# Performance work log

Hardware: AMD Instinct MI355X
Metric: run time of the kernel (lower is better)

The kernel has to match this reference:

```python
import jax, jax.numpy as jnp
import numpy as np

TOP_K = 2


def setup_inputs() -> dict:
    key = jax.random.key(0)
    ks = jax.random.split(key, 6)
    B, S, D, H, E = 2, 2048, 1024, 4096, 8
    s_in = 1.0 / np.sqrt(D)
    s_hid = 1.0 / np.sqrt(H)
    return {
        "x": jax.random.normal(ks[0], (B, S, D), jnp.float32),
        "Wg": jax.random.normal(ks[1], (E, D), jnp.float32) * s_in,
        "W1": jax.random.normal(ks[2], (E, D, H), jnp.float32) * s_in,
        "b1": jax.random.normal(ks[3], (E, H), jnp.float32) * 0.01,
        "W2": jax.random.normal(ks[4], (E, H, D), jnp.float32) * s_hid,
        "b2": jax.random.normal(ks[5], (E, D), jnp.float32) * 0.01,
    }


def reference(x, Wg, W1, b1, W2, b2):
    B, S, D = x.shape
    E = Wg.shape[0]
    T = B * S
    xf = x.reshape(T, D)

    # ---- router ----
    logits = xf @ Wg.T                              # (T, E)
    probs = jax.nn.softmax(logits, axis=-1)
    top_v, top_i = jax.lax.top_k(probs, TOP_K)      # (T, k)
    top_v = top_v / top_v.sum(axis=-1, keepdims=True)

    # aux load-balancing loss
    expert_mask = jax.nn.one_hot(top_i, E, dtype=probs.dtype).sum(axis=1)  # (T, E)
    f = expert_mask.mean(axis=0)
    p = probs.mean(axis=0)
    aux_loss = E * (f * p).sum()

    # ---- combine weights: scatter normalized top-k probs into (T, E) ----
    w = jnp.zeros((T, E), probs.dtype).at[jnp.arange(T)[:, None], top_i].add(top_v)

    # ---- all-expert FFN (grouped GEMM form), weighted combine ----
    h = jax.nn.silu(jnp.einsum('td,edh->teh', xf, W1) + b1[None])   # (T, E, H)
    y = jnp.einsum('teh,ehd->ted', h, W2) + b2[None]                # (T, E, D)
    out = jnp.einsum('ted,te->td', y, w)                            # (T, D)
    return out.reshape(B, S, D), aux_loss
```

## Files before the change

### kernel.cpp

```cpp
#include <hip/hip_runtime.h>
#include <cstdint>
#include <cstddef>

#define T_TOK 4096
#define DIM   1024
#define HID   4096
#define NE    8
#define PAD   128
#define PADMAX 9216

typedef _Float16 half_t;
typedef __attribute__((ext_vector_type(8))) _Float16 half8;
typedef __attribute__((ext_vector_type(4))) float floatx4;

__device__ __forceinline__ float silu_f(float v) {
  return v / (1.0f + expf(-v));
}

__device__ __forceinline__ half8 cvt44(float4 a, float4 b) {
  half8 o;
  o[0] = (half_t)a.x; o[1] = (half_t)a.y; o[2] = (half_t)a.z; o[3] = (half_t)a.w;
  o[4] = (half_t)b.x; o[5] = (half_t)b.y; o[6] = (half_t)b.z; o[7] = (half_t)b.w;
  return o;
}

__device__ __forceinline__ void gload16(const void* g, void* l) {
  __builtin_amdgcn_global_load_lds(
      (const __attribute__((address_space(1))) unsigned int*)g,
      (__attribute__((address_space(3))) unsigned int*)l, 16, 0, 0);
}

__global__ void k_reset(float* prob_sum, unsigned* cnt, unsigned* cursor,
                        int* pair_tok, float* pair_wt) {
  int i = blockIdx.x * 256 + threadIdx.x;
  if (i < PADMAX) { pair_tok[i] = 0; pair_wt[i] = 0.0f; }
  if (i < NE) { prob_sum[i] = 0.0f; cnt[i] = 0u; cursor[i] = 0u; }
}

__global__ __launch_bounds__(256) void k_cvt_x(const float* __restrict__ x,
                                               half_t* __restrict__ xh) {
  size_t i = (size_t)blockIdx.x * 256 + threadIdx.x;
  const float4* s = (const float4*)(x + i * 8);
  float4 a = s[0], b = s[1];
  *(half8*)(xh + i * 8) = cvt44(a, b);
}

__global__ __launch_bounds__(256) void k_tr_w1(const float* __restrict__ W1,
                                               half_t* __restrict__ W1t,
                                               int j0, int Hc) {
  __shared__ half_t T[64][72];
  int e = blockIdx.z, h0 = blockIdx.x * 64, d0 = blockIdx.y * 64;
  int tid = threadIdx.x;
  {
    int r = tid >> 2, c16 = (tid & 3) * 16;
    const float* s = W1 + ((size_t)e * DIM + d0 + r) * HID + j0 + h0 + c16;
    float4 a = ((const float4*)s)[0], b = ((const float4*)s)[1];
    float4 c = ((const float4*)s)[2], d = ((const float4*)s)[3];
    *(half8*)&T[r][c16] = cvt44(a, b);
    *(half8*)&T[r][c16 + 8] = cvt44(c, d);
  }
  __syncthreads();
  {
    int n = tid >> 2, d16 = (tid & 3) * 16;
    half8 u, v;
#pragma unroll
    for (int j = 0; j < 8; ++j) { u[j] = T[d16 + j][n]; v[j] = T[d16 + 8 + j][n]; }
    half_t* dst = W1t + ((size_t)e * Hc + h0 + n) * DIM + d0 + d16;
    *(half8*)dst = u;
    *(half8*)(dst + 8) = v;
  }
}

__global__ __launch_bounds__(256) void k_tr_w2(const float* __restrict__ W2,
                                               half_t* __restrict__ W2t,
                                               int j0, int Hc) {
  __shared__ half_t T[64][72];
  int e = blockIdx.z, d0 = blockIdx.x * 64, h0 = blockIdx.y * 64;
  int tid = threadIdx.x;
  {
    int r = tid >> 2, c16 = (tid & 3) * 16;
    const float* s = W2 + ((size_t)e * HID + j0 + h0 + r) * DIM + d0 + c16;
    float4 a = ((const float4*)s)[0], b = ((const float4*)s)[1];
    float4 c = ((const float4*)s)[2], d = ((const float4*)s)[3];
    *(half8*)&T[r][c16] = cvt44(a, b);
    *(half8*)&T[r][c16 + 8] = cvt44(c, d);
  }
  __syncthreads();
  {
    int n = tid >> 2, h16 = (tid & 3) * 16;
    half8 u, v;
#pragma unroll
    for (int j = 0; j < 8; ++j) { u[j] = T[h16 + j][n]; v[j] = T[h16 + 8 + j][n]; }
    half_t* dst = W2t + ((size_t)e * DIM + d0 + n) * Hc + h0 + h16;
    *(half8*)dst = u;
    *(half8*)(dst + 8) = v;
  }
}

__global__ __launch_bounds__(256) void k_router(
    const float* __restrict__ x, const float* __restrict__ Wg,
    int* __restrict__ top_i, float* __restrict__ top_w,
    float* __restrict__ prob_sum, unsigned* __restrict__ cnt) {
  __shared__ float sWg[NE * DIM];
  __shared__ float sProb[NE];
  __shared__ unsigned sCnt[NE];
  int tid = threadIdx.x;
  if (tid < NE) { sProb[tid] = 0.0f; sCnt[tid] = 0u; }
  for (int i = tid; i < NE * DIM; i += 256) sWg[i] = Wg[i];
  __syncthreads();

  int wave = tid >> 6, lane = tid & 63;
  for (int it = 0; it < 4; ++it) {
    int t = blockIdx.x * 16 + wave * 4 + it;
    const float* xp = x + (size_t)t * DIM;
    float acc[NE];
#pragma unroll
    for (int e = 0; e < NE; ++e) acc[e] = 0.0f;
    for (int i = 0; i < DIM / 64; ++i) {
      int d = i * 64 + lane;
      float xd = xp[d];
#pragma unroll
      for (int e = 0; e < NE; ++e) acc[e] = fmaf(xd, sWg[e * DIM + d], acc[e]);
    }
#pragma unroll
    for (int off = 32; off > 0; off >>= 1)
#pragma unroll
      for (int e = 0; e < NE; ++e) acc[e] += __shfl_xor(acc[e], off, 64);

    if (lane == 0) {
      float m = acc[0];
#pragma unroll
      for (int e = 1; e < NE; ++e) m = fmaxf(m, acc[e]);
      float pr[NE]; float s = 0.0f;
#pragma unroll
      for (int e = 0; e < NE; ++e) { pr[e] = expf(acc[e] - m); s += pr[e]; }
      float inv = 1.0f / s;
#pragma unroll
      for (int e = 0; e < NE; ++e) pr[e] *= inv;
      int i0 = 0; float v0 = pr[0];
#pragma unroll
      for (int e = 1; e < NE; ++e) if (pr[e] > v0) { v0 = pr[e]; i0 = e; }
      int i1 = -1; float v1 = -1.0f;
#pragma unroll
      for (int e = 0; e < NE; ++e) if (e != i0 && pr[e] > v1) { v1 = pr[e]; i1 = e; }
      float wn = 1.0f / (v0 + v1);
      top_i[t * 2 + 0] = i0; top_i[t * 2 + 1] = i1;
      top_w[t * 2 + 0] = v0 * wn; top_w[t * 2 + 1] = v1 * wn;
#pragma unroll
      for (int e = 0; e < NE; ++e) atomicAdd(&sProb[e], pr[e]);
      atomicAdd(&sCnt[i0], 1u);
      atomicAdd(&sCnt[i1], 1u);
    }
  }
  __syncthreads();
  if (tid < NE) {
    atomicAdd(&prob_sum[tid], sProb[tid]);
    atomicAdd(&cnt[tid], sCnt[tid]);
  }
}

__global__ void k_scan(const unsigned* __restrict__ cnt,
                       const float* __restrict__ prob_sum,
                       int* __restrict__ pad_off, int* __restrict__ ptotal,
                       float* __restrict__ aux_out) {
  if (threadIdx.x == 0 && blockIdx.x == 0) {
    int off = 0; float aux = 0.0f;
    for (int e = 0; e < NE; ++e) {
      pad_off[e] = off;
      off += (int)((cnt[e] + (PAD - 1u)) & ~(unsigned)(PAD - 1));
      aux += ((float)cnt[e] / (float)T_TOK) * (prob_sum[e] / (float)T_TOK);
    }
    pad_off[NE] = off;
    *ptotal = off;
    *aux_out = (float)NE * aux;
  }
}

__global__ void k_scatter(const int* __restrict__ top_i, const float* __restrict__ top_w,
                          const int* __restrict__ pad_off, unsigned* __restrict__ cursor,
                          int* __restrict__ pair_tok, float* __restrict__ pair_wt) {
  int t = blockIdx.x * 256 + threadIdx.x;
  if (t >= T_TOK) return;
#pragma unroll
  for (int k = 0; k < 2; ++k) {
    int e = top_i[t * 2 + k];
    unsigned pos = atomicAdd(&cursor[e], 1u);
    int idx = pad_off[e] + (int)pos;
    pair_tok[idx] = t;
    pair_wt[idx]  = top_w[t * 2 + k];
  }
}

__global__ void k_init_out(const int* __restrict__ top_i, const float* __restrict__ top_w,
                           const float* __restrict__ b2, float* __restrict__ out) {
  int idx = blockIdx.x * 256 + threadIdx.x;
  int t = idx >> 10, d = idx & (DIM - 1);
  int e0 = top_i[t * 2 + 0], e1 = top_i[t * 2 + 1];
  out[idx] = top_w[t * 2 + 0] * b2[e0 * DIM + d] + top_w[t * 2 + 1] * b2[e1 * DIM + d];
}

__global__ __launch_bounds__(256) void k_gemm1_a(
    const half_t* __restrict__ xh, const half_t* __restrict__ W1t,
    const float* __restrict__ b1, const int* __restrict__ pair_tok,
    const int* __restrict__ pad_off, const int* __restrict__ ptotal,
    half_t* __restrict__ hout, int j0, int Hc) {
  __shared__ half_t lds[16384];
  int P = *ptotal;
  int p0 = blockIdx.y * 128;
  if (p0 >= P) return;
  int e = 0;
#pragma unroll
  for (int q = 1; q < NE; ++q) if (p0 >= pad_off[q]) e = q;

  int tid = threadIdx.x, w = tid >> 6, l = tid & 63;
  int lr = l & 15, lq = l >> 4;
  int wr = w >> 1, wc = w & 1;
  int jt = blockIdx.x * 128;

  int tok0 = pair_tok[p0 + (2 * w) * 16 + lr];
  int tok1 = pair_tok[p0 + (2 * w + 1) * 16 + lr];
  const half_t* gA0 = xh + (size_t)tok0 * DIM + lq * 8;
  const half_t* gA1 = xh + (size_t)tok1 * DIM + lq * 8;
  const half_t* gB0 = W1t + ((size_t)e * Hc + jt + (2 * w) * 16 + lr) * DIM + lq * 8;
  const half_t* gB1 = W1t + ((size_t)e * Hc + jt + (2 * w + 1) * 16 + lr) * DIM + lq * 8;

  half_t* ldsA = lds;
  half_t* ldsB = lds + 8192;
  half_t* dA = ldsA + (4 * w) * 512;
  half_t* dB = ldsB + (4 * w) * 512;

  floatx4 acc[4][4];
#pragma unroll
  for (int i = 0; i < 4; ++i)
#pragma unroll
    for (int j = 0; j < 4; ++j) acc[i][j] = (floatx4){0.f, 0.f, 0.f, 0.f};

  for (int kt = 0; kt < DIM; kt += 64) {
    __syncthreads();
    gload16(gA0 + kt,      dA + 0 * 512);
    gload16(gA0 + kt + 32, dA + 1 * 512);
    gload16(gA1 + kt,      dA + 2 * 512);
    gload16(gA1 + kt + 32, dA + 3 * 512);
    gload16(gB0 + kt,      dB + 0 * 512);
    gload16(gB0 + kt + 32, dB + 1 * 512);
    gload16(gB1 + kt,      dB + 2 * 512);
    gload16(gB1 + kt + 32, dB + 3 * 512);
    __syncthreads();
#pragma unroll
    for (int ks = 0; ks < 2; ++ks) {
      half8 a[4], b[4];
#pragma unroll
      for (int i = 0; i < 4; ++i)
        a[i] = *(const half8*)(ldsA + ((4 * wr + i) * 2 + ks) * 512 + l * 8);
#pragma unroll
      for (int j = 0; j < 4; ++j)
        b[j] = *(const half8*)(ldsB + ((4 * wc + j) * 2 + ks) * 512 + l * 8);
#pragma unroll
      for (int i = 0; i < 4; ++i)
#pragma unroll
        for (int j = 0; j < 4; ++j)
          acc[i][j] = __builtin_amdgcn_mfma_f32_16x16x32_f16(a[i], b[j], acc[i][j], 0, 0, 0);
    }
  }
  __syncthreads();

#pragma unroll
  for (int j = 0; j < 4; ++j) {
    int coll = (4 * wc + j) * 16 + lr;
    float bias = b1[(size_t)e * HID + j0 + jt + coll];
#pragma unroll
    for (int i = 0; i < 4; ++i)
#pragma unroll
      for (int r = 0; r < 4; ++r) {
        int row = (4 * wr + i) * 16 + lq * 4 + r;
        lds[row * 128 + coll] = (half_t)silu_f(acc[i][j][r] + bias);
      }
  }
  __syncthreads();
#pragma unroll
  for (int ps = 0; ps < 4; ++ps) {
    int r = ps * 32 + (tid >> 3), c = (tid & 7) * 16;
    half8 v0 = *(const half8*)(lds + r * 128 + c);
    half8 v1 = *(const half8*)(lds + r * 128 + c + 8);
    half_t* dst = hout + (size_t)(p0 + r) * Hc + jt + c;
    *(half8*)dst = v0;
    *(half8*)(dst + 8) = v1;
  }
}

__global__ __launch_bounds__(256) void k_gemm2_a(
    const half_t* __restrict__ hbuf, const half_t* __restrict__ W2t,
    const int* __restrict__ pair_tok, const float* __restrict__ pair_wt,
    const int* __restrict__ pad_off, const int* __restrict__ ptotal,
    float* __restrict__ out, int Hc) {
  __shared__ half_t lds[16384];
  int P = *ptotal;
  int p0 = blockIdx.y * 128;
  if (p0 >= P) return;
  int e = 0;
#pragma unroll
  for (int q = 1; q < NE; ++q) if (p0 >= pad_off[q]) e = q;

  int tid = threadIdx.x, w = tid >> 6, l = tid & 63;
  int lr = l & 15, lq = l >> 4;
  int wr = w >> 1, wc = w & 1;
  int jt = blockIdx.x * 128;

  const half_t* gA0 = hbuf + (size_t)(p0 + (2 * w) * 16 + lr) * Hc + lq * 8;
  const half_t* gA1 = hbuf + (size_t)(p0 + (2 * w + 1) * 16 + lr) * Hc + lq * 8;
  const half_t* gB0 = W2t + ((size_t)e * DIM + jt + (2 * w) * 16 + lr) * Hc + lq * 8;
  const half_t* gB1 = W2t + ((size_t)e * DIM + jt + (2 * w + 1) * 16 + lr) * Hc + lq * 8;

  half_t* ldsA = lds;
  half_t* ldsB = lds + 8192;
  half_t* dA = ldsA + (4 * w) * 512;
  half_t* dB = ldsB + (4 * w) * 512;

  floatx4 acc[4][4];
#pragma unroll
  for (int i = 0; i < 4; ++i)
#pragma unroll
    for (int j = 0; j < 4; ++j) acc[i][j] = (floatx4){0.f, 0.f, 0.f, 0.f};

  for (int kt = 0; kt < Hc; kt += 64) {
    __syncthreads();
    gload16(gA0 + kt,      dA + 0 * 512);
    gload16(gA0 + kt + 32, dA + 1 * 512);
    gload16(gA1 + kt,      dA + 2 * 512);
    gload16(gA1 + kt + 32, dA + 3 * 512);
    gload16(gB0 + kt,      dB + 0 * 512);
    gload16(gB0 + kt + 32, dB + 1 * 512);
    gload16(gB1 + kt,      dB + 2 * 512);
    gload16(gB1 + kt + 32, dB + 3 * 512);
    __syncthreads();
#pragma unroll
    for (int ks = 0; ks < 2; ++ks) {
      half8 a[4], b[4];
#pragma unroll
      for (int i = 0; i < 4; ++i)
        a[i] = *(const half8*)(ldsA + ((4 * wr + i) * 2 + ks) * 512 + l * 8);
#pragma unroll
      for (int j = 0; j < 4; ++j)
        b[j] = *(const half8*)(ldsB + ((4 * wc + j) * 2 + ks) * 512 + l * 8);
#pragma unroll
      for (int i = 0; i < 4; ++i)
#pragma unroll
        for (int j = 0; j < 4; ++j)
          acc[i][j] = __builtin_amdgcn_mfma_f32_16x16x32_f16(a[i], b[j], acc[i][j], 0, 0, 0);
    }
  }

#pragma unroll
  for (int i = 0; i < 4; ++i)
#pragma unroll
    for (int r = 0; r < 4; ++r) {
      int row = (4 * wr + i) * 16 + lq * 4 + r;
      float wt = pair_wt[p0 + row];
      if (wt != 0.0f) {
        int tok = pair_tok[p0 + row];
        float* op = out + (size_t)tok * DIM + jt;
#pragma unroll
        for (int j = 0; j < 4; ++j) {
          int coll = (4 * wc + j) * 16 + lr;
          unsafeAtomicAdd(op + coll, wt * acc[i][j][r]);
        }
      }
    }
}

__global__ __launch_bounds__(256) void k_gemm1_b(
    const half_t* __restrict__ xh, const float* __restrict__ W1,
    const float* __restrict__ b1, const int* __restrict__ pair_tok,
    const int* __restrict__ pad_off, const int* __restrict__ ptotal,
    half_t* __restrict__ hout, int j0, int Hc) {
  __shared__ half_t lds[16384];
  int P = *ptotal;
  int p0 = blockIdx.y * 128;
  if (p0 >= P) return;
  int e = 0;
#pragma unroll
  for (int q = 1; q < NE; ++q) if (p0 >= pad_off[q]) e = q;

  int tid = threadIdx.x, w = tid >> 6, l = tid & 63;
  int lr = l & 15, lq = l >> 4;
  int wr = w >> 1, wc = w & 1;
  int jt = blockIdx.x * 128;

  int tok0 = pair_tok[p0 + (2 * w) * 16 + lr];
  int tok1 = pair_tok[p0 + (2 * w + 1) * 16 + lr];
  const half_t* gA0 = xh + (size_t)tok0 * DIM + lq * 8;
  const half_t* gA1 = xh + (size_t)tok1 * DIM + lq * 8;
  const float* gBb = W1 + (size_t)e * DIM * HID + j0 + jt;
  const float* gB0 = gBb + (2 * w) * 16 + lr;
  const float* gB1 = gBb + (2 * w + 1) * 16 + lr;

  half_t* ldsA = lds;
  half_t* ldsB = lds + 8192;

  floatx4 acc[4][4];
#pragma unroll
  for (int i = 0; i < 4; ++i)
#pragma unroll
    for (int j = 0; j < 4; ++j) acc[i][j] = (floatx4){0.f, 0.f, 0.f, 0.f};

  for (int kt = 0; kt < DIM; kt += 64) {
    half8 va0 = *(const half8*)(gA0 + kt);
    half8 va1 = *(const half8*)(gA0 + kt + 32);
    half8 va2 = *(const half8*)(gA1 + kt);
    half8 va3 = *(const half8*)(gA1 + kt + 32);
    half8 vb[4];
#pragma unroll
    for (int fg = 0; fg < 4; ++fg) {
      const float* gb = (fg >> 1) ? gB1 : gB0;
      int kbase = kt + (fg & 1) * 32 + lq * 8;
#pragma unroll
      for (int j = 0; j < 8; ++j)
        vb[fg][j] = (half_t)gb[(size_t)(kbase + j) * HID];
    }
    __syncthreads();
    *(half8*)(ldsA + (4 * w + 0) * 512 + l * 8) = va0;
    *(half8*)(ldsA + (4 * w + 1) * 512 + l * 8) = va1;
    *(half8*)(ldsA + (4 * w + 2) * 512 + l * 8) = va2;
    *(half8*)(ldsA + (4 * w + 3) * 512 + l * 8) = va3;
    *(half8*)(ldsB + (4 * w + 0) * 512 + l * 8) = vb[0];
    *(half8*)(ldsB + (4 * w + 1) * 512 + l * 8) = vb[1];
    *(half8*)(ldsB + (4 * w + 2) * 512 + l * 8) = vb[2];
    *(half8*)(ldsB + (4 * w + 3) * 512 + l * 8) = vb[3];
    __syncthreads();
#pragma unroll
    for (int ks = 0; ks < 2; ++ks) {
      half8 a[4], b[4];
#pragma unroll
      for (int i = 0; i < 4; ++i)
        a[i] = *(const half8*)(ldsA + ((4 * wr + i) * 2 + ks) * 512 + l * 8);
#pragma unroll
      for (int j = 0; j < 4; ++j)
        b[j] = *(const half8*)(ldsB + ((4 * wc + j) * 2 + ks) * 512 + l * 8);
#pragma unroll
      for (int i = 0; i < 4; ++i)
#pragma unroll
        for (int j = 0; j < 4; ++j)
          acc[i][j] = __builtin_amdgcn_mfma_f32_16x16x32_f16(a[i], b[j], acc[i][j], 0, 0, 0);
    }
  }
  __syncthreads();

#pragma unroll
  for (int j = 0; j < 4; ++j) {
    int coll = (4 * wc + j) * 16 + lr;
    float bias = b1[(size_t)e * HID + j0 + jt + coll];
#pragma unroll
    for (int i = 0; i < 4; ++i)
#pragma unroll
      for (int r = 0; r < 4; ++r) {
        int row = (4 * wr + i) * 16 + lq * 4 + r;
        lds[row * 128 + coll] = (half_t)silu_f(acc[i][j][r] + bias);
      }
  }
  __syncthreads();
#pragma unroll
  for (int ps = 0; ps < 4; ++ps) {
    int r = ps * 32 + (tid >> 3), c = (tid & 7) * 16;
    half8 v0 = *(const half8*)(lds + r * 128 + c);
    half8 v1 = *(const half8*)(lds + r * 128 + c + 8);
    half_t* dst = hout + (size_t)(p0 + r) * Hc + jt + c;
    *(half8*)dst = v0;
    *(half8*)(dst + 8) = v1;
  }
}

__global__ __launch_bounds__(256) void k_gemm2_b(
    const half_t* __restrict__ hbuf, const float* __restrict__ W2,
    const int* __restrict__ pair_tok, const float* __restrict__ pair_wt,
    const int* __restrict__ pad_off, const int* __restrict__ ptotal,
    float* __restrict__ out, int j0, int Hc) {
  __shared__ half_t lds[16384];
  int P = *ptotal;
  int p0 = blockIdx.y * 128;
  if (p0 >= P) return;
  int e = 0;
#pragma unroll
  for (int q = 1; q < NE; ++q) if (p0 >= pad_off[q]) e = q;

  int tid = threadIdx.x, w = tid >> 6, l = tid & 63;
  int lr = l & 15, lq = l >> 4;
  int wr = w >> 1, wc = w & 1;
  int jt = blockIdx.x * 128;

  const half_t* gA0 = hbuf + (size_t)(p0 + (2 * w) * 16 + lr) * Hc + lq * 8;
  const half_t* gA1 = hbuf + (size_t)(p0 + (2 * w + 1) * 16 + lr) * Hc + lq * 8;
  const float* gBb = W2 + (size_t)e * HID * DIM + jt;
  const float* gB0 = gBb + (2 * w) * 16 + lr;
  const float* gB1 = gBb + (2 * w + 1) * 16 + lr;

  half_t* ldsA = lds;
  half_t* ldsB = lds + 8192;

  floatx4 acc[4][4];
#pragma unroll
  for (int i = 0; i < 4; ++i)
#pragma unroll
    for (int j = 0; j < 4; ++j) acc[i][j] = (floatx4){0.f, 0.f, 0.f, 0.f};

  for (int kt = 0; kt < Hc; kt += 64) {
    half8 va0 = *(const half8*)(gA0 + kt);
    half8 va1 = *(const half8*)(gA0 + kt + 32);
    half8 va2 = *(const half8*)(gA1 + kt);
    half8 va3 = *(const half8*)(gA1 + kt + 32);
    half8 vb[4];
#pragma unroll
    for (int fg = 0; fg < 4; ++fg) {
      const float* gb = (fg >> 1) ? gB1 : gB0;
      int kbase = j0 + kt + (fg & 1) * 32 + lq * 8;
#pragma unroll
      for (int j = 0; j < 8; ++j)
        vb[fg][j] = (half_t)gb[(size_t)(kbase + j) * DIM];
    }
    __syncthreads();
    *(half8*)(ldsA + (4 * w + 0) * 512 + l * 8) = va0;
    *(half8*)(ldsA + (4 * w + 1) * 512 + l * 8) = va1;
    *(half8*)(ldsA + (4 * w + 2) * 512 + l * 8) = va2;
    *(half8*)(ldsA + (4 * w + 3) * 512 + l * 8) = va3;
    *(half8*)(ldsB + (4 * w + 0) * 512 + l * 8) = vb[0];
    *(half8*)(ldsB + (4 * w + 1) * 512 + l * 8) = vb[1];
    *(half8*)(ldsB + (4 * w + 2) * 512 + l * 8) = vb[2];
    *(half8*)(ldsB + (4 * w + 3) * 512 + l * 8) = vb[3];
    __syncthreads();
#pragma unroll
    for (int ks = 0; ks < 2; ++ks) {
      half8 a[4], b[4];
#pragma unroll
      for (int i = 0; i < 4; ++i)
        a[i] = *(const half8*)(ldsA + ((4 * wr + i) * 2 + ks) * 512 + l * 8);
#pragma unroll
      for (int j = 0; j < 4; ++j)
        b[j] = *(const half8*)(ldsB + ((4 * wc + j) * 2 + ks) * 512 + l * 8);
#pragma unroll
      for (int i = 0; i < 4; ++i)
#pragma unroll
        for (int j = 0; j < 4; ++j)
          acc[i][j] = __builtin_amdgcn_mfma_f32_16x16x32_f16(a[i], b[j], acc[i][j], 0, 0, 0);
    }
  }

#pragma unroll
  for (int i = 0; i < 4; ++i)
#pragma unroll
    for (int r = 0; r < 4; ++r) {
      int row = (4 * wr + i) * 16 + lq * 4 + r;
      float wt = pair_wt[p0 + row];
      if (wt != 0.0f) {
        int tok = pair_tok[p0 + row];
        float* op = out + (size_t)tok * DIM + jt;
#pragma unroll
        for (int j = 0; j < 4; ++j) {
          int coll = (4 * wc + j) * 16 + lr;
          unsafeAtomicAdd(op + coll, wt * acc[i][j][r]);
        }
      }
    }
}

extern "C" void kernel_launch(void* const* d_in, const int* in_sizes, int n_in,
                              void* d_out, int out_size, void* d_ws, size_t ws_size,
                              hipStream_t stream) {
  const float* x  = (const float*)d_in[0];
  const float* Wg = (const float*)d_in[1];
  const float* W1 = (const float*)d_in[2];
  const float* b1 = (const float*)d_in[3];
  const float* W2 = (const float*)d_in[4];
  const float* b2 = (const float*)d_in[5];
  float* out = (float*)d_out;

  char* p = (char*)d_ws;
  auto alloc = [&](size_t bytes) -> char* {
    char* r = p; p += (bytes + 255) & ~(size_t)255; return r;
  };
  int*      top_i    = (int*)     alloc((size_t)T_TOK * 2 * sizeof(int));
  float*    top_w    = (float*)   alloc((size_t)T_TOK * 2 * sizeof(float));
  float*    prob_sum = (float*)   alloc(NE * sizeof(float));
  unsigned* cnt      = (unsigned*)alloc(NE * sizeof(unsigned));
  int*      pad_off  = (int*)     alloc((NE + 1) * sizeof(int));
  int*      ptotal   = (int*)     alloc(sizeof(int));
  unsigned* cursor   = (unsigned*)alloc(NE * sizeof(unsigned));
  int*      pair_tok = (int*)     alloc(PADMAX * sizeof(int));
  float*    pair_wt  = (float*)   alloc(PADMAX * sizeof(float));
  half_t*   xh       = (half_t*)  alloc((size_t)T_TOK * DIM * sizeof(half_t));

  size_t used  = (size_t)(p - (char*)d_ws);
  size_t avail = ws_size > used ? ws_size - used : 0;

  size_t per_col_a = (size_t)2 * NE * DIM * sizeof(half_t) + (size_t)PADMAX * sizeof(half_t);
  int HcA = (int)((avail / per_col_a) & ~(size_t)127);
  if (HcA > HID) HcA = HID;
  bool modeA = (HcA >= 128);

  k_reset<<<dim3((PADMAX + 255) / 256), 256, 0, stream>>>(prob_sum, cnt, cursor, pair_tok, pair_wt);
  k_cvt_x<<<dim3((size_t)T_TOK * DIM / 8 / 256), 256, 0, stream>>>(x, xh);
  k_router<<<dim3(T_TOK / 16), 256, 0, stream>>>(x, Wg, top_i, top_w, prob_sum, cnt);
  k_scan<<<1, 64, 0, stream>>>(cnt, prob_sum, pad_off, ptotal, out + (size_t)T_TOK * DIM);
  k_scatter<<<dim3(T_TOK / 256), 256, 0, stream>>>(top_i, top_w, pad_off, cursor, pair_tok, pair_wt);
  k_init_out<<<dim3((size_t)T_TOK * DIM / 256), 256, 0, stream>>>(top_i, top_w, b2, out);

  if (modeA) {
    int Hc = HcA;
    half_t* W1t  = (half_t*)alloc((size_t)NE * Hc * DIM * sizeof(half_t));
    half_t* W2t  = (half_t*)alloc((size_t)NE * DIM * Hc * sizeof(half_t));
    half_t* hbuf = (half_t*)alloc((size_t)PADMAX * Hc * sizeof(half_t));
    for (int jb = 0; jb < HID; jb += Hc) {
      int hc = (HID - jb) < Hc ? (HID - jb) : Hc;
      k_tr_w1<<<dim3(hc / 64, DIM / 64, NE), 256, 0, stream>>>(W1, W1t, jb, hc);
      k_gemm1_a<<<dim3(hc / 128, PADMAX / 128), 256, 0, stream>>>(
          xh, W1t, b1, pair_tok, pad_off, ptotal, hbuf, jb, hc);
      k_tr_w2<<<dim3(DIM / 64, hc / 64, NE), 256, 0, stream>>>(W2, W2t, jb, hc);
      k_gemm2_a<<<dim3(DIM / 128, PADMAX / 128), 256, 0, stream>>>(
          hbuf, W2t, pair_tok, pair_wt, pad_off, ptotal, out, hc);
    }
  } else {
    int Hc = (int)((avail / ((size_t)PADMAX * sizeof(half_t))) & ~(size_t)127);
    if (Hc > HID) Hc = HID;
    if (Hc < 128) Hc = 128;
    half_t* hbuf = (half_t*)alloc((size_t)PADMAX * Hc * sizeof(half_t));
    for (int jb = 0; jb < HID; jb += Hc) {
      int hc = (HID - jb) < Hc ? (HID - jb) : Hc;
      k_gemm1_b<<<dim3(hc / 128, PADMAX / 128), 256, 0, stream>>>(
          xh, W1, b1, pair_tok, pad_off, ptotal, hbuf, jb, hc);
      k_gemm2_b<<<dim3(DIM / 128, PADMAX / 128), 256, 0, stream>>>(
          hbuf, W2, pair_tok, pair_wt, pad_off, ptotal, out, jb, hc);
    }
  }
}
```

Before: 756.8 us.

## Split-K gemm2 and remap blocks across XCDs for both expert GEMMs

Flattens the 2D grids of both grouped GEMMs into 1D, using an XCD-aware swizzle so consecutive logical tiles land on the same chiplet and share L2. The second GEMM also gets a 4-way K split over the hidden dimension to raise block count, since its grid was only 8 column tiles by up to 72 row tiles. It already accumulates with atomics, so the split adds more atomic traffic on the output. The swizzle assumes the grid size is divisible by 8.

```diff
diff --git a/kernel.cpp b/kernel.cpp
--- a/kernel.cpp
+++ b/kernel.cpp
@@ -8,6 +8,7 @@
 #define NE    8
 #define PAD   128
 #define PADMAX 9216
+#define KSPLIT2 4
 
 typedef _Float16 half_t;
 typedef __attribute__((ext_vector_type(8))) _Float16 half8;
@@ -28,6 +29,11 @@
   __builtin_amdgcn_global_load_lds(
       (const __attribute__((address_space(1))) unsigned int*)g,
       (__attribute__((address_space(3))) unsigned int*)l, 16, 0, 0);
+}
+
+__device__ __forceinline__ int xcd_swz(int lin, int Nw) {
+  int q = Nw >> 3;
+  return (lin & 7) * q + (lin >> 3);
 }
 
 __global__ void k_reset(float* prob_sum, unsigned* cnt, unsigned* cursor,
@@ -205,8 +211,11 @@
     const int* __restrict__ pad_off, const int* __restrict__ ptotal,
     half_t* __restrict__ hout, int j0, int Hc) {
   __shared__ half_t lds[16384];
+  int wid = xcd_swz(blockIdx.x, gridDim.x);
+  int col = wid / (PADMAX / 128);
+  int row = wid % (PADMAX / 128);
   int P = *ptotal;
-  int p0 = blockIdx.y * 128;
+  int p0 = row * 128;
   if (p0 >= P) return;
   int e = 0;
 #pragma unroll
@@ -215,7 +224,7 @@
   int tid = threadIdx.x, w = tid >> 6, l = tid & 63;
   int lr = l & 15, lq = l >> 4;
   int wr = w >> 1, wc = w & 1;
-  int jt = blockIdx.x * 128;
+  int jt = col * 128;
 
   int tok0 = pair_tok[p0 + (2 * w) * 16 + lr];
   int tok1 = pair_tok[p0 + (2 * w + 1) * 16 + lr];
@@ -272,8 +281,8 @@
     for (int i = 0; i < 4; ++i)
 #pragma unroll
       for (int r = 0; r < 4; ++r) {
-        int row = (4 * wr + i) * 16 + lq * 4 + r;
-        lds[row * 128 + coll] = (half_t)silu_f(acc[i][j][r] + bias);
+        int row2 = (4 * wr + i) * 16 + lq * 4 + r;
+        lds[row2 * 128 + coll] = (half_t)silu_f(acc[i][j][r] + bias);
       }
   }
   __syncthreads();
@@ -294,8 +303,13 @@
     const int* __restrict__ pad_off, const int* __restrict__ ptotal,
     float* __restrict__ out, int Hc) {
   __shared__ half_t lds[16384];
+  int wid = xcd_swz(blockIdx.x, gridDim.x);
+  int c  = wid & 7;
+  int rz = wid >> 3;
+  int row = rz % (PADMAX / 128);
+  int zk  = rz / (PADMAX / 128);
   int P = *ptotal;
-  int p0 = blockIdx.y * 128;
+  int p0 = row * 128;
   if (p0 >= P) return;
   int e = 0;
 #pragma unroll
@@ -304,7 +318,11 @@
   int tid = threadIdx.x, w = tid >> 6, l = tid & 63;
   int lr = l & 15, lq = l >> 4;
   int wr = w >> 1, wc = w & 1;
-  int jt = blockIdx.x * 128;
+  int jt = c * 128;
+
+  int ks_total = Hc >> 6;
+  int kt_beg = ((zk * ks_total) / KSPLIT2) * 64;
+  int kt_end = (((zk + 1) * ks_total) / KSPLIT2) * 64;
 
   const half_t* gA0 = hbuf + (size_t)(p0 + (2 * w) * 16 + lr) * Hc + lq * 8;
   const half_t* gA1 = hbuf + (size_t)(p0 + (2 * w + 1) * 16 + lr) * Hc + lq * 8;
@@ -322,7 +340,7 @@
 #pragma unroll
     for (int j = 0; j < 4; ++j) acc[i][j] = (floatx4){0.f, 0.f, 0.f, 0.f};
 
-  for (int kt = 0; kt < Hc; kt += 64) {
+  for (int kt = kt_beg; kt < kt_end; kt += 64) {
     __syncthreads();
     gload16(gA0 + kt,      dA + 0 * 512);
     gload16(gA0 + kt + 32, dA + 1 * 512);
@@ -354,10 +372,10 @@
   for (int i = 0; i < 4; ++i)
 #pragma unroll
     for (int r = 0; r < 4; ++r) {
-      int row = (4 * wr + i) * 16 + lq * 4 + r;
-      float wt = pair_wt[p0 + row];
+      int row2 = (4 * wr + i) * 16 + lq * 4 + r;
+      float wt = pair_wt[p0 + row2];
       if (wt != 0.0f) {
-        int tok = pair_tok[p0 + row];
+        int tok = pair_tok[p0 + row2];
         float* op = out + (size_t)tok * DIM + jt;
 #pragma unroll
         for (int j = 0; j < 4; ++j) {
@@ -610,10 +628,10 @@
     for (int jb = 0; jb < HID; jb += Hc) {
       int hc = (HID - jb) < Hc ? (HID - jb) : Hc;
       k_tr_w1<<<dim3(hc / 64, DIM / 64, NE), 256, 0, stream>>>(W1, W1t, jb, hc);
-      k_gemm1_a<<<dim3(hc / 128, PADMAX / 128), 256, 0, stream>>>(
+      k_gemm1_a<<<dim3((hc / 128) * (PADMAX / 128)), 256, 0, stream>>>(
           xh, W1t, b1, pair_tok, pad_off, ptotal, hbuf, jb, hc);
       k_tr_w2<<<dim3(DIM / 64, hc / 64, NE), 256, 0, stream>>>(W2, W2t, jb, hc);
-      k_gemm2_a<<<dim3(DIM / 128, PADMAX / 128), 256, 0, stream>>>(
+      k_gemm2_a<<<dim3((DIM / 128) * (PADMAX / 128) * KSPLIT2), 256, 0, stream>>>(
           hbuf, W2t, pair_tok, pair_wt, pad_off, ptotal, out, hc);
     }
   } else {
```

After: 748.3 us. No clear change (-1.1%).
